# Performance work log

Hardware: AMD Instinct MI355X
Metric: run time of the kernel (lower is better)

The kernel has to match this reference:

```python
import jax, jax.numpy as jnp
import numpy as np
from math import sqrt


def _init_linear(key, fan_in, fan_out, bias_fill=None):
    kw, kb = jax.random.split(key)
    s = 1.0 / np.sqrt(fan_in)
    W = jax.random.uniform(kw, (fan_in, fan_out), minval=-s, maxval=s, dtype=jnp.float32)
    if bias_fill is None:
        b = jax.random.uniform(kb, (fan_out,), minval=-s, maxval=s, dtype=jnp.float32)
    else:
        b = jnp.full((fan_out,), bias_fill, dtype=jnp.float32)
    return W, b


def setup_inputs() -> dict:
    key = jax.random.key(0)
    ks = jax.random.split(key, 16)
    N, P = 16, 4096
    C, H, W = 128, 28, 28
    G = 512  # global encoding dim
    inp = {}
    inp['points'] = jax.random.normal(ks[0], (N, P, 3), dtype=jnp.float32)
    inp['transform'] = 0.1 * jax.random.normal(ks[1], (N, P, 12), dtype=jnp.float32)
    inp['enc_filters'] = jax.random.normal(ks[2], (N, C, H, W), dtype=jnp.float32)
    inp['enc_glob'] = jax.random.normal(ks[3], (N, G), dtype=jnp.float32)
    # spat_mlp: 15 -> 128 -> 784 (one hidden layer)
    inp['sw1'], inp['sb1'] = _init_linear(ks[4], 3 + 12, 128)
    inp['sw2'], inp['sb2'] = _init_linear(ks[5], 128, H * W)
    # gate_mlp: 527 -> 128 -> 128, last bias init to 1
    inp['gw1'], inp['gb1'] = _init_linear(ks[6], G + 3 + 12, 128)
    inp['gw2'], inp['gb2'] = _init_linear(ks[7], 128, C, bias_fill=1.0)
    # fold mlp: 657 -> 128 -> 128 -> 3 (two hidden layers)
    D_in = C + G + 3 + 2 + 12
    inp['fw1'], inp['fb1'] = _init_linear(ks[8], D_in, 128)
    inp['fw2'], inp['fb2'] = _init_linear(ks[9], 128, 128)
    inp['fw3'], inp['fb3'] = _init_linear(ks[10], 128, 3)
    return inp


def _spatial_grid(k):
    # k x k grid in [-1, 1]^2, flattened to (k*k, 2)
    xs = jnp.linspace(-1.0, 1.0, k, dtype=jnp.float32)
    gx, gy = jnp.meshgrid(xs, xs, indexing='ij')
    return jnp.stack([gx.ravel(), gy.ravel()], axis=-1)


def _normalize_points(p):
    # center each cloud and scale to the unit sphere (max norm = 1)
    c = p - jnp.mean(p, axis=1, keepdims=True)
    scale = jnp.max(jnp.linalg.norm(c, axis=-1), axis=1, keepdims=True)  # (N,1)
    return c / (scale[..., None] + 1e-8)


def reference(points, transform, enc_filters, enc_glob,
              sw1, sb1, sw2, sb2, gw1, gb1, gw2, gb2,
              fw1, fb1, fw2, fb2, fw3, fb3):
    N, P, _ = points.shape
    _, C, H, W = enc_filters.shape
    G = enc_glob.shape[-1]
    factor = 1
    k = int(sqrt(P * factor))
    coords = jnp.broadcast_to(_spatial_grid(k)[None], (N, P * factor, 2))
    globs = jnp.broadcast_to(enc_glob[:, None, :], (N, P, G))
    code_vecs = jnp.concatenate([points, transform, globs], axis=-1)  # (N,P,527)
    # factor == 1 so repeat_interleave is identity
    fold_feats = jnp.concatenate([code_vecs, coords], axis=-1)  # (N,P,529)
    spat_in = fold_feats[:, :, : 3 + 12]
    gate_in = fold_feats[:, :, : 3 + 12 + G]
    # spatial attention over HW locations
    sh = jax.nn.relu(spat_in @ sw1 + sb1)
    sattn = jax.nn.softmax(sh @ sw2 + sb2, axis=-1)  # (N,P,HW)
    # channel gate
    gh = jax.nn.relu(gate_in @ gw1 + gb1)
    gattn = jax.nn.sigmoid(gh @ gw2 + gb2)  # (N,P,C)
    filters = enc_filters.reshape(N, C, H * W)
    spat_map = jnp.einsum('npq,ncq->npc', sattn, filters)  # fused weighted sum
    spat_feats = gattn * spat_map  # (N,P,C)
    inputs = jnp.concatenate([fold_feats, spat_feats], axis=-1)  # (N,P,657)
    h = jax.nn.relu(inputs @ fw1 + fb1)
    h = jax.nn.relu(h @ fw2 + fb2)
    deform = h @ fw3 + fb3  # (N,P,3)
    return _normalize_points(deform + inputs[:, :, :3])
```

## Files before the change

### kernel.cpp

```cpp
#include <hip/hip_runtime.h>
#include <hip/hip_bf16.h>

#define N_   16
#define P_   4096
#define C_   128
#define HW_  784
#define G_   512

typedef unsigned short u16;
typedef unsigned int   u32;
typedef __attribute__((ext_vector_type(8))) short bf16x8;
typedef __attribute__((ext_vector_type(4))) float f32x4;

union B8 { bf16x8 v; u32 w[4]; };

#define MFMA(a,b,c) __builtin_amdgcn_mfma_f32_16x16x32_bf16((a),(b),(c),0,0,0)

__device__ __forceinline__ u16 f2b(float f) {
    __hip_bfloat16 h = __float2bfloat16(f);
    return *reinterpret_cast<u16*>(&h);
}
__device__ __forceinline__ u32 pk(float lo, float hi) {
    return (u32)f2b(lo) | ((u32)f2b(hi) << 16);
}

#define OFF_SW2P    0
#define OFF_SW1P    204800
#define OFF_GW1P    212992
#define OFF_GW2P    221184
#define OFF_FW1BP   253952
#define OFF_FW2P    286720
#define OFF_SB2P    319488
#define OFF_GLOBGH  322688
#define OFF_GLOBF1  330880
#define OFF_FW1SP   339072
#define OFF_FW3P    347264
#define OFF_FILTP   349312

#define E0 102400
#define E1 110592
#define E2 118784
#define E3 135168
#define E4 151552
#define E5 167936
#define E6 168736
#define E7 185120
#define E8 189216
#define E9 189728
#define E10 599328

__device__ __forceinline__ int perm_c(int row) {
    const int ct = row >> 4, r = row & 15;
    return 32 * (ct >> 1) + 8 * (r >> 2) + 4 * (ct & 1) + (r & 3);
}

__global__ __launch_bounds__(256) void k_prep(
    const float* __restrict__ sw1, const float* __restrict__ sw2,
    const float* __restrict__ sb2, const float* __restrict__ gw1,
    const float* __restrict__ gw2, const float* __restrict__ fw1,
    const float* __restrict__ fw2, const float* __restrict__ fw3,
    const float* __restrict__ filters, const float* __restrict__ enc_glob,
    u16* __restrict__ sw2p, u16* __restrict__ sw1p, u16* __restrict__ gw1p,
    u16* __restrict__ gw2p, u16* __restrict__ fw1bp, u16* __restrict__ fw2p,
    float* __restrict__ sb2p, u16* __restrict__ fw1sp, float* __restrict__ fw3p,
    u16* __restrict__ filtp,
    float* __restrict__ glob_gh, float* __restrict__ glob_f1)
{
    const int idx = blockIdx.x * 256 + threadIdx.x;
    if (idx < E0) {
        const int r_new = idx >> 7, c = idx & 127;
        const int kt = r_new >> 5, o = r_new & 31, h = (o >> 4) & 1, r = o & 15;
        const int q = kt * 32 + 8 * (r >> 2) + 4 * h + (r & 3);
        sw2p[idx] = (q < HW_) ? f2b(sw2[c * HW_ + q]) : (u16)0;
    } else if (idx < E1) {
        const int t = idx - E0;
        const int row = t >> 5, k = t & 31;
        const int c = perm_c(row);
        sw1p[t] = (k < 15) ? f2b(sw1[k * C_ + c]) : (u16)0;
    } else if (idx < E2) {
        const int t = idx - E1;
        const int row = t >> 5, k = t & 31;
        const int c = perm_c(row);
        gw1p[t] = (k < 15) ? f2b(gw1[k * C_ + c]) : (u16)0;
    } else if (idx < E3) {
        const int t = idx - E2;
        const int row = t >> 7, ci = t & 127;
        gw2p[t] = f2b(gw2[ci * C_ + perm_c(row)]);
    } else if (idx < E4) {
        const int t = idx - E3;
        const int row = t >> 7, ci = t & 127;
        fw1bp[t] = f2b(fw1[(529 + ci) * C_ + perm_c(row)]);
    } else if (idx < E5) {
        const int t = idx - E4;
        const int row = t >> 7, ci = t & 127;
        fw2p[t] = f2b(fw2[ci * C_ + perm_c(row)]);
    } else if (idx < E6) {
        const int q = idx - E5;
        sb2p[q] = (q < HW_) ? sb2[q] : -1e30f;
    } else if (idx < E7) {
        const int t = idx - E6;
        const int sub = t & 3, r = t >> 2;
        const int which = r >> 11, nn = (r >> 7) & 15, c = r & 127;
        const float* W = which ? fw1 : gw1;
        const float* gv = enc_glob + nn * G_ + sub * 128;
        const float* Wp = W + (15 + sub * 128) * C_ + c;
        float acc = 0.f;
        for (int k = 0; k < 128; ++k) acc += gv[k] * Wp[k * C_];
        acc += __shfl_xor(acc, 1);
        acc += __shfl_xor(acc, 2);
        if (sub == 0) (which ? glob_f1 : glob_gh)[nn * C_ + c] = acc;
    } else if (idx < E8) {
        const int t = idx - E7;
        const int row = t >> 5, k = t & 31;
        const int c = perm_c(row);
        float v = 0.f;
        if (k < 15)       v = fw1[k * C_ + c];
        else if (k == 15) v = fw1[527 * C_ + c];
        else if (k == 16) v = fw1[528 * C_ + c];
        fw1sp[t] = f2b(v);
    } else if (idx < E9) {
        const int t = idx - E8;
        const int row = t >> 2, j = t & 3;
        fw3p[t] = (j < 3) ? fw3[perm_c(row) * 3 + j] : 0.f;
    } else if (idx < E10) {
        const int t = idx - E9;
        const int nn = t / 25600;
        const int rr = t % 25600;
        const int row = rr / 200, qg = rr % 200;
        const int q0 = qg * 4;
        const int c = perm_c(row);
        u32 lo = 0u, hi = 0u;
        if (q0 < HW_) {
            const f32x4 v = *(const f32x4*)(filters + ((size_t)nn * C_ + c) * HW_ + q0);
            lo = pk(v[0], v[1]); hi = pk(v[2], v[3]);
        }
        const size_t base = (size_t)nn * 102400 + (size_t)row * 800 + q0;
        *(uint2*)(filtp + base) = make_uint2(lo, hi);
    }
}

__global__ __launch_bounds__(512, 2) void k_mfma(
    const float* __restrict__ points, const float* __restrict__ transform,
    const float* __restrict__ sb1, const float* __restrict__ gb1,
    const float* __restrict__ gb2, const float* __restrict__ fb1,
    const float* __restrict__ fb2, const float* __restrict__ fb3,
    const u16* __restrict__ sw1p, const u16* __restrict__ gw1p,
    const u16* __restrict__ sw2p, const float* __restrict__ sb2p,
    const u16* __restrict__ gw2p, const u16* __restrict__ fw1bp,
    const u16* __restrict__ fw2p, const u16* __restrict__ fw1sp,
    const float* __restrict__ fw3p, const u16* __restrict__ filtp,
    const float* __restrict__ glob_gh, const float* __restrict__ glob_f1,
    float* __restrict__ out)
{
    __shared__ __align__(16) float s_x[8][32][16];
    __shared__ __align__(16) u16 s_w[2][32][136];
    __shared__ __align__(16) u16 s_f[2][128][36];

    const int tid = threadIdx.x, wid = tid >> 6, lane = tid & 63;
    const int p = lane & 15, g = lane >> 4;
    const int bid = blockIdx.x;
    const int nb  = (bid & 7) * 32 + (bid >> 3);
    const int n   = nb >> 4;
    const int pw  = ((nb & 15) << 8) + (wid << 5);

    const u16* filtn = filtp + (size_t)n * 102400;
    const int swrow = tid >> 4, swc = tid & 15;
    const int frp   = tid >> 2, fc16 = tid & 3;

    for (int i = lane; i < 512; i += 64) {
        const int pt = i >> 4, k = i & 15;
        const int gp = n * P_ + pw + pt;
        float v = 0.f;
        if (k < 3)       v = points[gp * 3 + k];
        else if (k < 15) v = transform[gp * 12 + k - 3];
        s_x[wid][pt][k] = v;
    }

    {
        const bf16x8 w0 = *(const bf16x8*)(sw2p + (size_t)swrow * C_ + swc * 8);
        const bf16x8 f0 = *(const bf16x8*)(filtn + (size_t)frp * 800 + fc16 * 8);
        *(bf16x8*)&s_w[0][swrow][swc * 8] = w0;
        *(bf16x8*)&s_f[0][frp][fc16 * 8]  = f0;
    }
    __syncthreads();

    B8 bxc[2];
    #pragma unroll
    for (int f = 0; f < 2; ++f) {
        bxc[f].w[0] = bxc[f].w[1] = bxc[f].w[2] = bxc[f].w[3] = 0u;
        const float* xs = &s_x[wid][p + 16 * f][0];
        const int pp = pw + p + 16 * f;
        const float cx = -1.f + 2.f * (float)(pp >> 6) / 63.f;
        const float cy = -1.f + 2.f * (float)(pp & 63) / 63.f;
        if (g == 0) {
            bxc[f].w[0] = pk(xs[0], xs[1]);  bxc[f].w[1] = pk(xs[2], xs[3]);
            bxc[f].w[2] = pk(xs[4], xs[5]);  bxc[f].w[3] = pk(xs[6], xs[7]);
        } else if (g == 1) {
            bxc[f].w[0] = pk(xs[8], xs[9]);  bxc[f].w[1] = pk(xs[10], xs[11]);
            bxc[f].w[2] = pk(xs[12], xs[13]); bxc[f].w[3] = pk(xs[14], cx);
        } else if (g == 2) {
            bxc[f].w[0] = pk(cy, 0.f);
        }
    }

    B8 bsh[4][2];
    #pragma unroll
    for (int ct = 0; ct < 8; ++ct) {
        const bf16x8 a_s = *(const bf16x8*)(sw1p + (16 * ct + p) * 32 + 8 * g);
        const int cb = 32 * (ct >> 1) + 8 * g + 4 * (ct & 1);
        const f32x4 b1 = *(const f32x4*)(sb1 + cb);
        const int m = ct >> 1, o = (ct & 1) * 2;
        #pragma unroll
        for (int f = 0; f < 2; ++f) {
            f32x4 cs = (f32x4){0.f, 0.f, 0.f, 0.f};
            cs = MFMA(a_s, bxc[f].v, cs);
            const float s0 = fmaxf(cs[0] + b1[0], 0.f), s1 = fmaxf(cs[1] + b1[1], 0.f);
            const float s2 = fmaxf(cs[2] + b1[2], 0.f), s3 = fmaxf(cs[3] + b1[3], 0.f);
            bsh[m][f].w[o] = pk(s0, s1); bsh[m][f].w[o + 1] = pk(s2, s3);
        }
    }

    f32x4 pv[8][2];
    #pragma unroll
    for (int ct = 0; ct < 8; ++ct)
        #pragma unroll
        for (int f = 0; f < 2; ++f) pv[ct][f] = (f32x4){0.f, 0.f, 0.f, 0.f};
    float psum0 = 0.f, psum1 = 0.f;

    for (int kt = 0; kt < 25; ++kt) {
        const int cur = kt & 1, nxt = cur ^ 1;
        bf16x8 stw0, stf0;
        if (kt < 24) {
            const int q0 = 32 * (kt + 1);
            stw0 = *(const bf16x8*)(sw2p + (size_t)(q0 + swrow) * C_ + swc * 8);
            stf0 = *(const bf16x8*)(filtn + (size_t)frp * 800 + q0 + fc16 * 8);
        }

        B8 bq[2];
        #pragma unroll
        for (int h = 0; h < 2; ++h) {
            const u16* wr = &s_w[cur][16 * h + p][8 * g];
            const bf16x8 aw0 = *(const bf16x8*)(wr);
            const bf16x8 aw1 = *(const bf16x8*)(wr + 32);
            const bf16x8 aw2 = *(const bf16x8*)(wr + 64);
            const bf16x8 aw3 = *(const bf16x8*)(wr + 96);
            const f32x4 bi = *(const f32x4*)(sb2p + 32 * kt + 8 * g + 4 * h);
            #pragma unroll
            for (int f = 0; f < 2; ++f) {
                f32x4 c4 = (f32x4){0.f, 0.f, 0.f, 0.f};
                c4 = MFMA(aw0, bsh[0][f].v, c4);
                c4 = MFMA(aw1, bsh[1][f].v, c4);
                c4 = MFMA(aw2, bsh[2][f].v, c4);
                c4 = MFMA(aw3, bsh[3][f].v, c4);
                const float e0 = __expf(fminf(c4[0] + bi[0], 60.f));
                const float e1 = __expf(fminf(c4[1] + bi[1], 60.f));
                const float e2 = __expf(fminf(c4[2] + bi[2], 60.f));
                const float e3 = __expf(fminf(c4[3] + bi[3], 60.f));
                if (f == 0) psum0 += (e0 + e1) + (e2 + e3);
                else        psum1 += (e0 + e1) + (e2 + e3);
                bq[f].w[2 * h + 0] = pk(e0, e1);
                bq[f].w[2 * h + 1] = pk(e2, e3);
            }
        }
        #pragma unroll
        for (int ct = 0; ct < 8; ++ct) {
            const bf16x8 af = *(const bf16x8*)&s_f[cur][16 * ct + p][8 * g];
            pv[ct][0] = MFMA(af, bq[0].v, pv[ct][0]);
            pv[ct][1] = MFMA(af, bq[1].v, pv[ct][1]);
        }

        if (kt < 24) {
            *(bf16x8*)&s_w[nxt][swrow][swc * 8] = stw0;
            *(bf16x8*)&s_f[nxt][frp][fc16 * 8]  = stf0;
        }
        __syncthreads();
    }
    psum0 += __shfl_xor(psum0, 16); psum0 += __shfl_xor(psum0, 32);
    psum1 += __shfl_xor(psum1, 16); psum1 += __shfl_xor(psum1, 32);
    const float inv0 = 1.f / psum0, inv1 = 1.f / psum1;

    B8 bgh[4][2];
    #pragma unroll
    for (int ct = 0; ct < 8; ++ct) {
        const bf16x8 a_g = *(const bf16x8*)(gw1p + (16 * ct + p) * 32 + 8 * g);
        const int cb = 32 * (ct >> 1) + 8 * g + 4 * (ct & 1);
        const f32x4 b2 = *(const f32x4*)(gb1 + cb);
        const f32x4 gg = *(const f32x4*)(glob_gh + n * C_ + cb);
        const int m = ct >> 1, o = (ct & 1) * 2;
        #pragma unroll
        for (int f = 0; f < 2; ++f) {
            f32x4 cg = (f32x4){0.f, 0.f, 0.f, 0.f};
            cg = MFMA(a_g, bxc[f].v, cg);
            const float g0 = fmaxf(cg[0] + b2[0] + gg[0], 0.f), g1 = fmaxf(cg[1] + b2[1] + gg[1], 0.f);
            const float g2 = fmaxf(cg[2] + b2[2] + gg[2], 0.f), g3 = fmaxf(cg[3] + b2[3] + gg[3], 0.f);
            bgh[m][f].w[o] = pk(g0, g1); bgh[m][f].w[o + 1] = pk(g2, g3);
        }
    }

    B8 bsf[4][2];
    #pragma unroll
    for (int ct = 0; ct < 8; ++ct) {
        const u16* ar = gw2p + (16 * ct + p) * C_ + 8 * g;
        const bf16x8 a0 = *(const bf16x8*)(ar),      a1 = *(const bf16x8*)(ar + 32);
        const bf16x8 a2 = *(const bf16x8*)(ar + 64), a3 = *(const bf16x8*)(ar + 96);
        const int cb = 32 * (ct >> 1) + 8 * g + 4 * (ct & 1);
        const f32x4 gb = *(const f32x4*)(gb2 + cb);
        const int m = ct >> 1, o = (ct & 1) * 2;
        #pragma unroll
        for (int f = 0; f < 2; ++f) {
            f32x4 acc = (f32x4){0.f, 0.f, 0.f, 0.f};
            acc = MFMA(a0, bgh[0][f].v, acc);
            acc = MFMA(a1, bgh[1][f].v, acc);
            acc = MFMA(a2, bgh[2][f].v, acc);
            acc = MFMA(a3, bgh[3][f].v, acc);
            const float iv = f ? inv1 : inv0;
            const float s0 = pv[ct][f][0] * iv / (1.f + __expf(-(acc[0] + gb[0])));
            const float s1 = pv[ct][f][1] * iv / (1.f + __expf(-(acc[1] + gb[1])));
            const float s2 = pv[ct][f][2] * iv / (1.f + __expf(-(acc[2] + gb[2])));
            const float s3 = pv[ct][f][3] * iv / (1.f + __expf(-(acc[3] + gb[3])));
            bsf[m][f].w[o] = pk(s0, s1); bsf[m][f].w[o + 1] = pk(s2, s3);
        }
    }

    B8 bh1[4][2];
    #pragma unroll
    for (int ct = 0; ct < 8; ++ct) {
        const u16* ar = fw1bp + (16 * ct + p) * C_ + 8 * g;
        const bf16x8 a0 = *(const bf16x8*)(ar),      a1 = *(const bf16x8*)(ar + 32);
        const bf16x8 a2 = *(const bf16x8*)(ar + 64), a3 = *(const bf16x8*)(ar + 96);
        const bf16x8 a_s = *(const bf16x8*)(fw1sp + (16 * ct + p) * 32 + 8 * g);
        const int cb = 32 * (ct >> 1) + 8 * g + 4 * (ct & 1);
        const f32x4 fbv = *(const f32x4*)(fb1 + cb);
        const f32x4 gf  = *(const f32x4*)(glob_f1 + n * C_ + cb);
        const int m = ct >> 1, o = (ct & 1) * 2;
        #pragma unroll
        for (int f = 0; f < 2; ++f) {
            f32x4 acc = (f32x4){0.f, 0.f, 0.f, 0.f};
            acc = MFMA(a0, bsf[0][f].v, acc);
            acc = MFMA(a1, bsf[1][f].v, acc);
            acc = MFMA(a2, bsf[2][f].v, acc);
            acc = MFMA(a3, bsf[3][f].v, acc);
            acc = MFMA(a_s, bxc[f].v, acc);
            const float h0 = fmaxf(acc[0] + fbv[0] + gf[0], 0.f);
            const float h1v = fmaxf(acc[1] + fbv[1] + gf[1], 0.f);
            const float h2 = fmaxf(acc[2] + fbv[2] + gf[2], 0.f);
            const float h3 = fmaxf(acc[3] + fbv[3] + gf[3], 0.f);
            bh1[m][f].w[o] = pk(h0, h1v); bh1[m][f].w[o + 1] = pk(h2, h3);
        }
    }

    float d0[2] = {0.f, 0.f}, d1[2] = {0.f, 0.f}, d2[2] = {0.f, 0.f};
    #pragma unroll
    for (int ct = 0; ct < 8; ++ct) {
        const u16* ar = fw2p + (16 * ct + p) * C_ + 8 * g;
        const bf16x8 a0 = *(const bf16x8*)(ar),      a1 = *(const bf16x8*)(ar + 32);
        const bf16x8 a2 = *(const bf16x8*)(ar + 64), a3 = *(const bf16x8*)(ar + 96);
        const int cb = 32 * (ct >> 1) + 8 * g + 4 * (ct & 1);
        const f32x4 o4 = *(const f32x4*)(fb2 + cb);
        f32x4 w3r[4];
        #pragma unroll
        for (int r = 0; r < 4; ++r)
            w3r[r] = *(const f32x4*)(fw3p + (16 * ct + 4 * g + r) * 4);
        #pragma unroll
        for (int f = 0; f < 2; ++f) {
            f32x4 acc = (f32x4){0.f, 0.f, 0.f, 0.f};
            acc = MFMA(a0, bh1[0][f].v, acc);
            acc = MFMA(a1, bh1[1][f].v, acc);
            acc = MFMA(a2, bh1[2][f].v, acc);
            acc = MFMA(a3, bh1[3][f].v, acc);
            #pragma unroll
            for (int r = 0; r < 4; ++r) {
                const float h = fmaxf(acc[r] + o4[r], 0.f);
                d0[f] += h * w3r[r][0];
                d1[f] += h * w3r[r][1];
                d2[f] += h * w3r[r][2];
            }
        }
    }
    #pragma unroll
    for (int f = 0; f < 2; ++f) {
        float a0 = d0[f], a1 = d1[f], a2 = d2[f];
        a0 += __shfl_xor(a0, 16); a0 += __shfl_xor(a0, 32);
        a1 += __shfl_xor(a1, 16); a1 += __shfl_xor(a1, 32);
        a2 += __shfl_xor(a2, 16); a2 += __shfl_xor(a2, 32);
        if (g == 0) {
            const int pt = p + 16 * f;
            const int gp = n * P_ + pw + pt;
            out[gp * 3 + 0] = a0 + fb3[0] + s_x[wid][pt][0];
            out[gp * 3 + 1] = a1 + fb3[1] + s_x[wid][pt][1];
            out[gp * 3 + 2] = a2 + fb3[2] + s_x[wid][pt][2];
        }
    }
}

__global__ __launch_bounds__(1024) void k_norm(float* __restrict__ out)
{
    __shared__ float red[48];
    __shared__ float red2[16];
    const int n = blockIdx.x, tid = threadIdx.x;
    float* pb = out + (size_t)n * P_ * 3;

    float sx = 0.f, sy = 0.f, sz = 0.f;
    for (int i = tid; i < P_; i += 1024) {
        sx += pb[i * 3 + 0]; sy += pb[i * 3 + 1]; sz += pb[i * 3 + 2];
    }
    #pragma unroll
    for (int m = 32; m >= 1; m >>= 1) {
        sx += __shfl_xor(sx, m); sy += __shfl_xor(sy, m); sz += __shfl_xor(sz, m);
    }
    const int wv = tid >> 6, ln = tid & 63;
    if (ln == 0) { red[wv * 3 + 0] = sx; red[wv * 3 + 1] = sy; red[wv * 3 + 2] = sz; }
    __syncthreads();
    float meanx = 0.f, meany = 0.f, meanz = 0.f;
    #pragma unroll
    for (int w = 0; w < 16; ++w) {
        meanx += red[w * 3 + 0]; meany += red[w * 3 + 1]; meanz += red[w * 3 + 2];
    }
    meanx /= (float)P_; meany /= (float)P_; meanz /= (float)P_;

    float mm = 0.f;
    for (int i = tid; i < P_; i += 1024) {
        const float dx = pb[i * 3 + 0] - meanx;
        const float dy = pb[i * 3 + 1] - meany;
        const float dz = pb[i * 3 + 2] - meanz;
        mm = fmaxf(mm, dx * dx + dy * dy + dz * dz);
    }
    #pragma unroll
    for (int m = 32; m >= 1; m >>= 1) mm = fmaxf(mm, __shfl_xor(mm, m));
    if (ln == 0) red2[wv] = mm;
    __syncthreads();
    mm = 0.f;
    #pragma unroll
    for (int w = 0; w < 16; ++w) mm = fmaxf(mm, red2[w]);
    const float scale = 1.f / (sqrtf(mm) + 1e-8f);

    for (int i = tid; i < P_; i += 1024) {
        pb[i * 3 + 0] = (pb[i * 3 + 0] - meanx) * scale;
        pb[i * 3 + 1] = (pb[i * 3 + 1] - meany) * scale;
        pb[i * 3 + 2] = (pb[i * 3 + 2] - meanz) * scale;
    }
}

extern "C" void kernel_launch(void* const* d_in, const int* in_sizes, int n_in,
                              void* d_out, int out_size, void* d_ws, size_t ws_size,
                              hipStream_t stream) {
    const float* points    = (const float*)d_in[0];
    const float* transform = (const float*)d_in[1];
    const float* filters   = (const float*)d_in[2];
    const float* enc_glob  = (const float*)d_in[3];
    const float* sw1 = (const float*)d_in[4];
    const float* sb1 = (const float*)d_in[5];
    const float* sw2 = (const float*)d_in[6];
    const float* sb2 = (const float*)d_in[7];
    const float* gw1 = (const float*)d_in[8];
    const float* gb1 = (const float*)d_in[9];
    const float* gw2 = (const float*)d_in[10];
    const float* gb2 = (const float*)d_in[11];
    const float* fw1 = (const float*)d_in[12];
    const float* fb1 = (const float*)d_in[13];
    const float* fw2 = (const float*)d_in[14];
    const float* fb2 = (const float*)d_in[15];
    const float* fw3 = (const float*)d_in[16];
    const float* fb3 = (const float*)d_in[17];

    char* ws = (char*)d_ws;
    u16*   sw2p    = (u16*)(ws + OFF_SW2P);
    u16*   sw1p    = (u16*)(ws + OFF_SW1P);
    u16*   gw1p    = (u16*)(ws + OFF_GW1P);
    u16*   gw2p    = (u16*)(ws + OFF_GW2P);
    u16*   fw1bp   = (u16*)(ws + OFF_FW1BP);
    u16*   fw2p    = (u16*)(ws + OFF_FW2P);
    float* sb2p    = (float*)(ws + OFF_SB2P);
    float* glob_gh = (float*)(ws + OFF_GLOBGH);
    float* glob_f1 = (float*)(ws + OFF_GLOBF1);
    u16*   fw1sp   = (u16*)(ws + OFF_FW1SP);
    float* fw3p    = (float*)(ws + OFF_FW3P);
    u16*   filtp   = (u16*)(ws + OFF_FILTP);
    float* out     = (float*)d_out;

    k_prep<<<(E10 + 255) / 256, 256, 0, stream>>>(
        sw1, sw2, sb2, gw1, gw2, fw1, fw2, fw3, filters, enc_glob,
        sw2p, sw1p, gw1p, gw2p, fw1bp, fw2p, sb2p, fw1sp, fw3p, filtp,
        glob_gh, glob_f1);
    k_mfma<<<N_ * (P_ / 256), 512, 0, stream>>>(
        points, transform, sb1, gb1, gb2, fb1, fb2, fb3,
        sw1p, gw1p, sw2p, sb2p, gw2p, fw1bp, fw2p, fw1sp, fw3p, filtp,
        glob_gh, glob_f1, out);
    k_norm<<<N_, 1024, 0, stream>>>(out);
}
```

Before: 182.3 us.

## Deepen global prefetch to two chunks ahead and stage softmax bias in LDS

Restructures the 25-step softmax-attention loop into a 2x-unrolled form. Global loads for weight and filter tiles are now issued two chunks ahead using two register sets, so more memory latency can be hidden behind MFMA work, and the buffer indices become compile-time constants. The sb2 bias is copied into shared memory once per block instead of being read from global memory on every chunk. Holding the extra prefetch registers adds register pressure under the 512x2 launch bounds.

New measurement: 171.3 us. 6.0% less time.

```diff
diff --git a/kernel.cpp b/kernel.cpp
--- a/kernel.cpp
+++ b/kernel.cpp
@@ -155,6 +155,7 @@
     __shared__ __align__(16) float s_x[8][32][16];
     __shared__ __align__(16) u16 s_w[2][32][136];
     __shared__ __align__(16) u16 s_f[2][128][36];
+    __shared__ __align__(16) float s_b[800];
 
     const int tid = threadIdx.x, wid = tid >> 6, lane = tid & 63;
     const int p = lane & 15, g = lane >> 4;
@@ -181,7 +182,11 @@
         const bf16x8 f0 = *(const bf16x8*)(filtn + (size_t)frp * 800 + fc16 * 8);
         *(bf16x8*)&s_w[0][swrow][swc * 8] = w0;
         *(bf16x8*)&s_f[0][frp][fc16 * 8]  = f0;
-    }
+        if (tid < 200)
+            *(f32x4*)&s_b[tid * 4] = *(const f32x4*)(sb2p + tid * 4);
+    }
+    bf16x8 Aw = *(const bf16x8*)(sw2p + (size_t)(32 + swrow) * C_ + swc * 8);
+    bf16x8 Af = *(const bf16x8*)(filtn + (size_t)frp * 800 + 32 + fc16 * 8);
     __syncthreads();
 
     B8 bxc[2];
@@ -227,54 +232,67 @@
         for (int f = 0; f < 2; ++f) pv[ct][f] = (f32x4){0.f, 0.f, 0.f, 0.f};
     float psum0 = 0.f, psum1 = 0.f;
 
-    for (int kt = 0; kt < 25; ++kt) {
-        const int cur = kt & 1, nxt = cur ^ 1;
-        bf16x8 stw0, stf0;
-        if (kt < 24) {
-            const int q0 = 32 * (kt + 1);
-            stw0 = *(const bf16x8*)(sw2p + (size_t)(q0 + swrow) * C_ + swc * 8);
-            stf0 = *(const bf16x8*)(filtn + (size_t)frp * 800 + q0 + fc16 * 8);
-        }
-
-        B8 bq[2];
-        #pragma unroll
-        for (int h = 0; h < 2; ++h) {
-            const u16* wr = &s_w[cur][16 * h + p][8 * g];
-            const bf16x8 aw0 = *(const bf16x8*)(wr);
-            const bf16x8 aw1 = *(const bf16x8*)(wr + 32);
-            const bf16x8 aw2 = *(const bf16x8*)(wr + 64);
-            const bf16x8 aw3 = *(const bf16x8*)(wr + 96);
-            const f32x4 bi = *(const f32x4*)(sb2p + 32 * kt + 8 * g + 4 * h);
-            #pragma unroll
-            for (int f = 0; f < 2; ++f) {
-                f32x4 c4 = (f32x4){0.f, 0.f, 0.f, 0.f};
-                c4 = MFMA(aw0, bsh[0][f].v, c4);
-                c4 = MFMA(aw1, bsh[1][f].v, c4);
-                c4 = MFMA(aw2, bsh[2][f].v, c4);
-                c4 = MFMA(aw3, bsh[3][f].v, c4);
-                const float e0 = __expf(fminf(c4[0] + bi[0], 60.f));
-                const float e1 = __expf(fminf(c4[1] + bi[1], 60.f));
-                const float e2 = __expf(fminf(c4[2] + bi[2], 60.f));
-                const float e3 = __expf(fminf(c4[3] + bi[3], 60.f));
-                if (f == 0) psum0 += (e0 + e1) + (e2 + e3);
-                else        psum1 += (e0 + e1) + (e2 + e3);
-                bq[f].w[2 * h + 0] = pk(e0, e1);
-                bq[f].w[2 * h + 1] = pk(e2, e3);
-            }
-        }
-        #pragma unroll
-        for (int ct = 0; ct < 8; ++ct) {
-            const bf16x8 af = *(const bf16x8*)&s_f[cur][16 * ct + p][8 * g];
-            pv[ct][0] = MFMA(af, bq[0].v, pv[ct][0]);
-            pv[ct][1] = MFMA(af, bq[1].v, pv[ct][1]);
-        }
-
-        if (kt < 24) {
-            *(bf16x8*)&s_w[nxt][swrow][swc * 8] = stw0;
-            *(bf16x8*)&s_f[nxt][frp][fc16 * 8]  = stf0;
-        }
+#define COMPUTE_CHUNK(KT, BUF)                                                 \
+    do {                                                                       \
+        B8 bq[2];                                                              \
+        _Pragma("unroll")                                                      \
+        for (int h = 0; h < 2; ++h) {                                          \
+            const u16* wr = &s_w[BUF][16 * h + p][8 * g];                      \
+            const bf16x8 aw0 = *(const bf16x8*)(wr);                           \
+            const bf16x8 aw1 = *(const bf16x8*)(wr + 32);                      \
+            const bf16x8 aw2 = *(const bf16x8*)(wr + 64);                      \
+            const bf16x8 aw3 = *(const bf16x8*)(wr + 96);                      \
+            const f32x4 bi = *(const f32x4*)&s_b[32 * (KT) + 8 * g + 4 * h];   \
+            _Pragma("unroll")                                                  \
+            for (int f = 0; f < 2; ++f) {                                      \
+                f32x4 c4 = (f32x4){0.f, 0.f, 0.f, 0.f};                        \
+                c4 = MFMA(aw0, bsh[0][f].v, c4);                               \
+                c4 = MFMA(aw1, bsh[1][f].v, c4);                               \
+                c4 = MFMA(aw2, bsh[2][f].v, c4);                               \
+                c4 = MFMA(aw3, bsh[3][f].v, c4);                               \
+                const float e0 = __expf(fminf(c4[0] + bi[0], 60.f));           \
+                const float e1 = __expf(fminf(c4[1] + bi[1], 60.f));           \
+                const float e2 = __expf(fminf(c4[2] + bi[2], 60.f));           \
+                const float e3 = __expf(fminf(c4[3] + bi[3], 60.f));           \
+                if (f == 0) psum0 += (e0 + e1) + (e2 + e3);                    \
+                else        psum1 += (e0 + e1) + (e2 + e3);                    \
+                bq[f].w[2 * h + 0] = pk(e0, e1);                               \
+                bq[f].w[2 * h + 1] = pk(e2, e3);                               \
+            }                                                                  \
+        }                                                                      \
+        _Pragma("unroll")                                                      \
+        for (int ct = 0; ct < 8; ++ct) {                                       \
+            const bf16x8 af = *(const bf16x8*)&s_f[BUF][16 * ct + p][8 * g];   \
+            pv[ct][0] = MFMA(af, bq[0].v, pv[ct][0]);                          \
+            pv[ct][1] = MFMA(af, bq[1].v, pv[ct][1]);                          \
+        }                                                                      \
+    } while (0)
+
+    bf16x8 Bw, Bf;
+    for (int kt = 0; kt < 24; kt += 2) {
+        {
+            const int q0 = 32 * (kt + 2);
+            Bw = *(const bf16x8*)(sw2p + (size_t)(q0 + swrow) * C_ + swc * 8);
+            Bf = *(const bf16x8*)(filtn + (size_t)frp * 800 + q0 + fc16 * 8);
+        }
+        COMPUTE_CHUNK(kt, 0);
+        *(bf16x8*)&s_w[1][swrow][swc * 8] = Aw;
+        *(bf16x8*)&s_f[1][frp][fc16 * 8]  = Af;
         __syncthreads();
-    }
+
+        if (kt + 3 <= 24) {
+            const int q0 = 32 * (kt + 3);
+            Aw = *(const bf16x8*)(sw2p + (size_t)(q0 + swrow) * C_ + swc * 8);
+            Af = *(const bf16x8*)(filtn + (size_t)frp * 800 + q0 + fc16 * 8);
+        }
+        COMPUTE_CHUNK(kt + 1, 1);
+        *(bf16x8*)&s_w[0][swrow][swc * 8] = Bw;
+        *(bf16x8*)&s_f[0][frp][fc16 * 8]  = Bf;
+        __syncthreads();
+    }
+    COMPUTE_CHUNK(24, 0);
+#undef COMPUTE_CHUNK
+
     psum0 += __shfl_xor(psum0, 16); psum0 += __shfl_xor(psum0, 32);
     psum1 += __shfl_xor(psum1, 16); psum1 += __shfl_xor(psum1, 32);
     const float inv0 = 1.f / psum0, inv1 = 1.f / psum1;
```
